# Kernel tuning notes

Measured on AMD Instinct MI355X. Metric: run time of the kernel, lower is better.

Reference implementation:

```python
import jax, jax.numpy as jnp
import numpy as np

N, E, DN, DE, H, L = 2048, 32768, 512, 512, 8, 2
BN_EPS = 1e-5  # torch BatchNorm1d eps; eval mode with running_mean=0, running_var=1


def setup_inputs():
    key = jax.random.key(0)
    ks = jax.random.split(key, 12)
    rng = np.random.default_rng(0)
    # unique directed edges: 3E/4 upper-triangular pairs + reverses of the first E/4
    iu, ju = np.triu_indices(N, k=1)
    sel = rng.choice(iu.size, size=3 * E // 4, replace=False)
    s, d = iu[sel], ju[sel]
    src = np.concatenate([s, d[: E // 4]])
    dst = np.concatenate([d, s[: E // 4]])
    edge_index = jnp.asarray(np.stack([src, dst]).astype(np.int32))

    def p(k, shape, fan_in):
        return jax.random.normal(k, shape, jnp.float32) / np.sqrt(fan_in).astype(np.float32)

    return dict(
        x=jax.random.normal(ks[0], (N, DN), jnp.float32),
        edge_feature=jax.random.normal(ks[1], (E, DE), jnp.float32),
        node_pos=jax.random.uniform(ks[2], (N, 3), jnp.float32) * 10.0,
        inw=p(ks[3], (L, 3 * DN, DN), DN),          # MHA in_proj_weight per layer
        inb=jnp.zeros((L, 3 * DN), jnp.float32),
        ow=p(ks[4], (L, DN, DN), DN),               # MHA out_proj
        ob=jnp.zeros((L, DN), jnp.float32),
        etw=p(ks[5], (L, DE, DE), DE),              # edge_transform Linear
        etb=jnp.zeros((L, DE), jnp.float32),
        etg=jnp.ones((L, DE), jnp.float32),         # edge_transform BN gamma
        etbb=jnp.zeros((L, DE), jnp.float32),       # edge_transform BN beta
        unw=p(ks[6], (L, DN, DN + DE), DN + DE),    # update_node Linear
        unb=jnp.zeros((L, DN), jnp.float32),
        uew=p(ks[7], (L, DE, 2 * DN + 2 * DE), 2 * DN + 2 * DE),  # update_edge Linear
        ueb=jnp.zeros((L, DE), jnp.float32),
        edge_index=edge_index,
    )


def _forward(x, edge_feature, node_pos, inw, inb, ow, ob, etw, etb, etg, etbb, unw, unb, uew, ueb, edge_index):
    src, dst = edge_index[0], edge_index[1]
    n, e = x.shape[0], src.shape[0]
    hd = DN // H
    # vectorized reverse-edge lookup (mirrors the torch edge_dict)
    keys = src * n + dst
    rkeys = dst * n + src
    order = jnp.argsort(keys)
    sk = keys[order]
    pos = jnp.clip(jnp.searchsorted(sk, rkeys), 0, e - 1)
    found = sk[pos] == rkeys
    rev_idx = order[pos]
    # distance-based attention mask: -inf everywhere, 1/(dist+eps) on (symmetric) edges, 1.0 on diagonal
    diff = node_pos[src] - node_pos[dst]
    w = 1.0 / (jnp.sqrt(jnp.sum(diff * diff, axis=-1)) + 1e-6)
    mask = jnp.full((n, n), -jnp.inf, x.dtype)
    mask = mask.at[src, dst].set(w).at[dst, src].set(w)
    diag = jnp.arange(n)
    mask = mask.at[diag, diag].set(1.0)
    bn_scale = np.float32(1.0 / np.sqrt(1.0 + BN_EPS))
    nf, ef = x, edge_feature
    for l in range(L):
        rev = jnp.where(found[:, None], ef[rev_idx], 0.0)
        # MHSA over all nodes as one sequence (batch=1), eval mode (dropout off)
        qkv = nf @ inw[l].T + inb[l]
        q, k, v = [t.reshape(n, H, hd) for t in jnp.split(qkv, 3, axis=-1)]
        scores = jnp.einsum('nhd,mhd->hnm', q * np.float32(1.0 / np.sqrt(hd)), k) + mask
        attn = jax.nn.softmax(scores, axis=-1)
        ctx = jnp.einsum('hnm,mhd->nhd', attn, v).reshape(n, DN)
        x_upd = ctx @ ow[l].T + ob[l]
        # message: update_edge on [x_i, e, e_rev, x_j] (flow=target_to_source -> x_i = x[src])
        upd_edge = jnp.concatenate([nf[src], ef, rev, nf[dst]], axis=1) @ uew[l].T + ueb[l]
        # edge_transform = Linear + BN(eval) + ReLU
        te = jax.nn.relu((ef @ etw[l].T + etb[l]) * bn_scale * etg[l] + etbb[l])
        # scatter-max to subject/object nodes (empty segments -> 0, torch_scatter convention)
        subj = jax.ops.segment_max(te, src, num_segments=n)
        obj = jax.ops.segment_max(te, dst, num_segments=n)
        subj = jnp.where(jnp.isneginf(subj), 0.0, subj)
        obj = jnp.where(jnp.isneginf(obj), 0.0, obj)
        nf = jnp.concatenate([x_upd, subj + obj], axis=1) @ unw[l].T + unb[l]
        ef = upd_edge
        if l < L - 1 or L == 1:
            nf = jax.nn.relu(nf)
            ef = jax.nn.relu(ef)
    return nf, ef


def reference(x, edge_feature, node_pos, inw, inb, ow, ob, etw, etb, etg, etbb, unw, unb, uew, ueb, edge_index):
    return _forward(x, edge_feature, node_pos, inw, inb, ow, ob, etw, etb, etg, etbb, unw, unb, uew, ueb, edge_index)
```

## Files before the change

kernel.cpp:

```cpp
#include <hip/hip_runtime.h>
#include <hip/hip_bf16.h>

#define NN 2048
#define EE 32768
#define DND 512
#define NH 8
#define HD 64
#define MAXD 128
#define NEGF (-1e30f)
#define BN_SCALE 0.9999950000374997f

typedef __attribute__((ext_vector_type(8))) short bf16x8;
typedef __attribute__((ext_vector_type(4))) float f32x4;
typedef unsigned short u16;
typedef unsigned int u32;

static __device__ __forceinline__ float4 ld4(const float* p) {
    return *reinterpret_cast<const float4*>(p);
}
static __device__ __forceinline__ u16 f2b(float f) {
    __hip_bfloat16 h = __float2bfloat16(f);
    return *reinterpret_cast<u16*>(&h);
}
static __device__ __forceinline__ float b2f(u32 bits) {
    return __uint_as_float(bits << 16);
}
static __device__ __forceinline__ void gl_lds(const u16* g, u16* l) {
    __builtin_amdgcn_global_load_lds((const __attribute__((address_space(1))) void*)g,
                                     (__attribute__((address_space(3))) void*)l, 16, 0, 0);
}


__global__ __launch_bounds__(256) void setup_init_k(int* __restrict__ t,
                                                    int* __restrict__ adj, float* __restrict__ wadj,
                                                    int* __restrict__ cnt,
                                                    int* __restrict__ ocnt, int* __restrict__ icnt,
                                                    u16* __restrict__ zero)
{
    int i = blockIdx.x * 256 + threadIdx.x;
    t[i] = -1;
    if (i < NN) {
        cnt[i] = 1; adj[i * MAXD] = i; wadj[i * MAXD] = 1.0f;
        ocnt[i] = 0; icnt[i] = 0;
    }
    if (i < 1024) zero[i] = 0;
}

__global__ __launch_bounds__(256) void fill_scatter_k(const int* __restrict__ ei, int* __restrict__ t,
                                                      int* __restrict__ oadj, int* __restrict__ ocnt,
                                                      int* __restrict__ iadj, int* __restrict__ icnt)
{
    int e = blockIdx.x * 256 + threadIdx.x;
    if (e >= EE) return;
    int s = ei[e], d = ei[EE + e];
    t[(size_t)s * NN + d] = e;
    int slot = atomicAdd(&ocnt[s], 1);
    if (slot < MAXD) oadj[s * MAXD + slot] = e;
    slot = atomicAdd(&icnt[d], 1);
    if (slot < MAXD) iadj[d * MAXD + slot] = e;
}

__global__ __launch_bounds__(256) void rev_csr_k(const int* __restrict__ ei, const int* __restrict__ t,
                                                 const float* __restrict__ pos,
                                                 int* __restrict__ rev,
                                                 int* __restrict__ adj, float* __restrict__ wadj,
                                                 int* __restrict__ cnt)
{
    int e = blockIdx.x * 256 + threadIdx.x;
    if (e >= EE) return;
    int s = ei[e], d = ei[EE + e];
    int r = t[(size_t)d * NN + s];
    rev[e] = r;
    float dx = pos[s * 3 + 0] - pos[d * 3 + 0];
    float dy = pos[s * 3 + 1] - pos[d * 3 + 1];
    float dz = pos[s * 3 + 2] - pos[d * 3 + 2];
    float w = 1.0f / (sqrtf(dx * dx + dy * dy + dz * dz) + 1e-6f);
    int slot = atomicAdd(&cnt[s], 1);
    if (slot < MAXD) { adj[s * MAXD + slot] = d; wadj[s * MAXD + slot] = w; }
    if (r < 0) {
        slot = atomicAdd(&cnt[d], 1);
        if (slot < MAXD) { adj[d * MAXD + slot] = s; wadj[d * MAXD + slot] = w; }
    }
}

__global__ __launch_bounds__(256) void conv_all_k(
    const float* __restrict__ x, const float* __restrict__ inw, const float* __restrict__ ow,
    const float* __restrict__ etw, const float* __restrict__ unw, const float* __restrict__ uew,
    const float* __restrict__ efin, u16* __restrict__ dst)
{
    size_t i = ((size_t)blockIdx.x * 256 + threadIdx.x) * 8;
    const float* s;
    size_t off;
    if (i < 1048576)      { s = x;    off = i; }
    else if (i < 2621440) { s = inw;  off = i - 1048576; }
    else if (i < 3145728) { s = ow;   off = i - 2621440; }
    else if (i < 3670016) { s = etw;  off = i - 3145728; }
    else if (i < 4718592) { s = unw;  off = i - 3670016; }
    else if (i < 6815744) { s = uew;  off = i - 4718592; }
    else                  { s = efin; off = i - 6815744; }
    float4 a = ld4(s + off), b = ld4(s + off + 4);
    u16 o[8];
    o[0] = f2b(a.x); o[1] = f2b(a.y); o[2] = f2b(a.z); o[3] = f2b(a.w);
    o[4] = f2b(b.x); o[5] = f2b(b.y); o[6] = f2b(b.z); o[7] = f2b(b.w);
    *reinterpret_cast<int4*>(dst + i) = *reinterpret_cast<const int4*>(o);
}

__global__ __launch_bounds__(256) void gather_max_k(const u16* __restrict__ te,
                                                    const int* __restrict__ oadj, const int* __restrict__ ocnt,
                                                    const int* __restrict__ iadj, const int* __restrict__ icnt,
                                                    u16* __restrict__ sums)
{
    const int i = blockIdx.x;
    const int c2 = threadIdx.x;
    float ms0 = 0.f, ms1 = 0.f, mo0 = 0.f, mo1 = 0.f;
    int no = ocnt[i]; if (no > MAXD) no = MAXD;
    for (int s = 0; s < no; ++s) {
        const int e = oadj[i * MAXD + s];
        const u32 v = *reinterpret_cast<const u32*>(te + (size_t)e * DND + c2 * 2);
        ms0 = fmaxf(ms0, b2f(v & 0xffffu));
        ms1 = fmaxf(ms1, b2f(v >> 16));
    }
    int ni = icnt[i]; if (ni > MAXD) ni = MAXD;
    for (int s = 0; s < ni; ++s) {
        const int e = iadj[i * MAXD + s];
        const u32 v = *reinterpret_cast<const u32*>(te + (size_t)e * DND + c2 * 2);
        mo0 = fmaxf(mo0, b2f(v & 0xffffu));
        mo1 = fmaxf(mo1, b2f(v >> 16));
    }
    const u32 r = (u32)f2b(ms0 + mo0) | ((u32)f2b(ms1 + mo1) << 16);
    *reinterpret_cast<u32*>(sums + (size_t)i * DND + c2 * 2) = r;
}

template <int MODE, int EPI, int WF32, int WBF16, int GY>
__global__ __launch_bounds__(256) void mgemm_k(
    const u16* __restrict__ WS, u32 a_off, u32 b_off, const float* __restrict__ bias,
    float* __restrict__ Cf, u16* __restrict__ Cb, int M, int Nc, int K,
    u32 g0_off, u32 g1_off, u32 gz_off,
    const int* __restrict__ srcv, const int* __restrict__ dstv, const int* __restrict__ revv,
    const float* __restrict__ eg, const float* __restrict__ eb)
{
    __shared__ u16 As2[2][8192];
    __shared__ u16 Bs2[2][8192];
    const int tid = threadIdx.x, lane = tid & 63, w = tid >> 6;
    const int wr = w >> 1, wc = w & 1;
    const int b = blockIdx.x;
    const int xcd = b & 7, kb = b >> 3;
    const int bm = ((kb / GY) * 8 + xcd) * 128;
    const int bn = (kb % GY) * 128;

    const int rl = lane >> 3;
    const u32 lx = (u32)(((lane & 7) ^ rl) * 8);

    u32 offA0[4], offA1[4], offB[4];
#pragma unroll
    for (int q = 0; q < 4; ++q) {
        const int ra = bm + w * 32 + q * 8 + rl;
        if (MODE == 0) {
            offA0[q] = a_off + (u32)ra * (u32)K + lx;
        } else {
            offA0[q] = g0_off + (u32)ra * 512u + lx;
            offA1[q] = g1_off + (u32)ra * 512u + lx;
        }
        offB[q] = b_off + (u32)(bn + w * 32 + q * 8 + rl) * (u32)K + lx;
    }

    const int nks = K >> 6;
    const int kq = lane >> 4, li = lane & 15;

    auto stage = [&](int t, int buf) {
        const u32 k0 = (u32)t * 64u;
        const int seg = (MODE == 0) ? 0 : (int)(k0 >> 9);
#pragma unroll
        for (int q = 0; q < 4; ++q) {
            u32 oa = (MODE == 0) ? offA0[q] : (seg == 0 ? offA0[q] : offA1[q]);
            const u32 koff = (MODE == 0) ? k0 : (k0 & 511u);
            gl_lds(WS + oa + koff, &As2[buf][(w * 32 + q * 8) * 64]);
        }
#pragma unroll
        for (int q = 0; q < 4; ++q)
            gl_lds(WS + offB[q] + k0, &Bs2[buf][(w * 32 + q * 8) * 64]);
    };

    f32x4 acc[4][4] = {};
    const int baseA = (wr * 64 + li) * 64 + ((kq ^ (li & 7)) * 8);
    const int baseB = (wc * 64 + li) * 64 + ((kq ^ (li & 7)) * 8);

    stage(0, 0);
    for (int t = 0; t < nks; ++t) {
        const int cur = t & 1;
        if (t + 1 < nks) stage(t + 1, cur ^ 1);
        if (t + 1 < nks) asm volatile("s_waitcnt vmcnt(8)" ::: "memory");
        else             asm volatile("s_waitcnt vmcnt(0)" ::: "memory");
        __builtin_amdgcn_s_barrier();
        __builtin_amdgcn_sched_barrier(0);
#pragma unroll
        for (int sub = 0; sub < 2; ++sub) {
            const int sx = sub << 5;
            bf16x8 af[4], bf[4];
#pragma unroll
            for (int m = 0; m < 4; ++m)
                af[m] = *reinterpret_cast<const bf16x8*>(&As2[cur][(baseA + m * 1024) ^ sx]);
#pragma unroll
            for (int n = 0; n < 4; ++n)
                bf[n] = *reinterpret_cast<const bf16x8*>(&Bs2[cur][(baseB + n * 1024) ^ sx]);
#pragma unroll
            for (int m = 0; m < 4; ++m)
#pragma unroll
                for (int n = 0; n < 4; ++n)
                    acc[m][n] = __builtin_amdgcn_mfma_f32_16x16x32_bf16(af[m], bf[n], acc[m][n], 0, 0, 0);
        }
        __builtin_amdgcn_s_barrier();
        __builtin_amdgcn_sched_barrier(0);
    }

    float bsv[4], scv[4], shv[4];
#pragma unroll
    for (int n = 0; n < 4; ++n) {
        const int col = bn + wc * 64 + n * 16 + li;
        bsv[n] = bias[col];
        if (EPI == 2) { scv[n] = BN_SCALE * eg[col]; shv[n] = eb[col]; }
    }
#pragma unroll
    for (int m = 0; m < 4; ++m) {
#pragma unroll
        for (int n = 0; n < 4; ++n) {
            const int col = bn + wc * 64 + n * 16 + li;
#pragma unroll
            for (int i = 0; i < 4; ++i) {
                float v = acc[m][n][i] + bsv[n];
                if (EPI == 2) v = fmaxf(fmaf(v, scv[n], shv[n]), 0.f);
                else if (EPI == 1) v = fmaxf(v, 0.f);
                const int r = bm + wr * 64 + m * 16 + (lane >> 4) * 4 + i;
                if (WF32) Cf[(size_t)r * Nc + col] = v;
                if (WBF16) Cb[(size_t)r * Nc + col] = f2b(v);
            }
        }
    }
}

template <int MODE, int EPI, int WF32, int WBF16>
__global__ __launch_bounds__(512, 2) void mgemm256_k(
    const u16* __restrict__ WS, u32 a_off, u32 b_off, const float* __restrict__ bias,
    float* __restrict__ Cf, u16* __restrict__ Cb, int M, int Nc, int K,
    u32 g0_off, u32 g1_off, u32 gz_off,
    const int* __restrict__ srcv, const int* __restrict__ dstv, const int* __restrict__ revv,
    const float* __restrict__ eg, const float* __restrict__ eb)
{
    __shared__ u16 SB[65536];
    const int tid = threadIdx.x, lane = tid & 63, w = tid >> 6;
    const int wr = w >> 2, wc = w & 3;
    const int b = blockIdx.x;
    const int bm = ((b & 7) + 8 * (b >> 4)) * 256;
    const int bn = ((b >> 3) & 1) * 256;

    const int rl = lane >> 3;
    const u32 lx = (u32)(((lane & 7) ^ rl) * 8);

    u32 offA0[4], offA1[4], offA2[4], offA3[4], offB[4];
#pragma unroll
    for (int q = 0; q < 4; ++q) {
        const int ra = bm + w * 32 + q * 8 + rl;
        if (MODE == 0) {
            offA0[q] = a_off + (u32)ra * (u32)K + lx;
        } else {
            offA0[q] = g0_off + (u32)srcv[ra] * 512u + lx;
            offA1[q] = g1_off + (u32)ra * 512u + lx;
            const int rv = revv[ra];
            offA2[q] = (rv >= 0 ? g1_off + (u32)rv * 512u : gz_off) + lx;
            offA3[q] = g0_off + (u32)dstv[ra] * 512u + lx;
        }
        offB[q] = b_off + (u32)(bn + w * 32 + q * 8 + rl) * (u32)K + lx;
    }

    const int nks = K >> 6;
    const int kq = lane >> 4, li = lane & 15;

    auto stageA2 = [&](int t, int buf, int q0) {
        const u32 k0 = (u32)t * 64u;
        const int seg = (MODE == 0) ? 0 : (int)(k0 >> 9);
        const u32 koff = (MODE == 0) ? k0 : (k0 & 511u);
#pragma unroll
        for (int q = q0; q < q0 + 2; ++q) {
            u32 oa;
            if (MODE == 0) oa = offA0[q];
            else           oa = (seg == 0 ? offA0[q] : seg == 1 ? offA1[q] : seg == 2 ? offA2[q] : offA3[q]);
            gl_lds(WS + oa + koff, &SB[buf * 16384 + (w * 32 + q * 8) * 64]);
        }
    };
    auto stageB2 = [&](int t, int buf, int q0) {
        const u32 k0 = (u32)t * 64u;
#pragma unroll
        for (int q = q0; q < q0 + 2; ++q)
            gl_lds(WS + offB[q] + k0, &SB[32768 + buf * 16384 + (w * 32 + q * 8) * 64]);
    };

    f32x4 acc[8][4] = {};
    const int baseA = (wr * 128 + li) * 64 + ((kq ^ (li & 7)) * 8);
    const int baseB = (wc * 64 + li) * 64 + ((kq ^ (li & 7)) * 8);

    stageA2(0, 0, 0); stageA2(0, 0, 2); stageB2(0, 0, 0); stageB2(0, 0, 2);
    for (int t = 0; t < nks; ++t) {
        const int cur = t & 1;
        const bool pf = (t + 1 < nks);
        if (pf) {
            stageA2(t + 1, cur ^ 1, 0);
            asm volatile("s_waitcnt vmcnt(2)" ::: "memory");
        } else {
            asm volatile("s_waitcnt vmcnt(0)" ::: "memory");
        }
        __builtin_amdgcn_s_barrier();
        __builtin_amdgcn_sched_barrier(0);
#pragma unroll
        for (int sub = 0; sub < 2; ++sub) {
            const int sx = sub << 5;
            bf16x8 bf[4];
#pragma unroll
            for (int n = 0; n < 4; ++n)
                bf[n] = *reinterpret_cast<const bf16x8*>(&SB[(32768 + cur * 16384 + baseB + n * 1024) ^ sx]);
#pragma unroll
            for (int mh = 0; mh < 2; ++mh) {
                if (pf) {
                    if (sub == 0 && mh == 0)      stageA2(t + 1, cur ^ 1, 2);
                    else if (sub == 0 && mh == 1) stageB2(t + 1, cur ^ 1, 0);
                    else if (sub == 1 && mh == 0) stageB2(t + 1, cur ^ 1, 2);
                }
                bf16x8 af[4];
#pragma unroll
                for (int m = 0; m < 4; ++m)
                    af[m] = *reinterpret_cast<const bf16x8*>(&SB[(cur * 16384 + baseA + (mh * 4 + m) * 1024) ^ sx]);
                __builtin_amdgcn_sched_barrier(0);
                __builtin_amdgcn_s_setprio(1);
#pragma unroll
                for (int m = 0; m < 4; ++m)
#pragma unroll
                    for (int n = 0; n < 4; ++n)
                        acc[mh * 4 + m][n] =
                            __builtin_amdgcn_mfma_f32_16x16x32_bf16(af[m], bf[n], acc[mh * 4 + m][n], 0, 0, 0);
                __builtin_amdgcn_s_setprio(0);
                __builtin_amdgcn_sched_barrier(0);
            }
        }
        __builtin_amdgcn_s_barrier();
        __builtin_amdgcn_sched_barrier(0);
    }

    float bsv[4], scv[4], shv[4];
#pragma unroll
    for (int n = 0; n < 4; ++n) {
        const int col = bn + wc * 64 + n * 16 + li;
        bsv[n] = bias[col];
        if (EPI == 2) { scv[n] = BN_SCALE * eg[col]; shv[n] = eb[col]; }
    }
#pragma unroll
    for (int m = 0; m < 8; ++m) {
#pragma unroll
        for (int n = 0; n < 4; ++n) {
            const int col = bn + wc * 64 + n * 16 + li;
#pragma unroll
            for (int i = 0; i < 4; ++i) {
                float v = acc[m][n][i] + bsv[n];
                if (EPI == 2) v = fmaxf(fmaf(v, scv[n], shv[n]), 0.f);
                else if (EPI == 1) v = fmaxf(v, 0.f);
                const int r = bm + wr * 128 + m * 16 + (lane >> 4) * 4 + i;
                if (WF32) Cf[(size_t)r * Nc + col] = v;
                if (WBF16) Cb[(size_t)r * Nc + col] = f2b(v);
            }
        }
    }
}

__global__ __launch_bounds__(256) void attn_sp_k(const u16* __restrict__ qkvb,
                                                 const int* __restrict__ adj,
                                                 const float* __restrict__ wadj,
                                                 const int* __restrict__ cnt,
                                                 u16* __restrict__ ctxb)
{
    const int i = blockIdx.x;
    const int wv = threadIdx.x >> 6, lane = threadIdx.x & 63;
    const int h = blockIdx.y * 4 + wv;
    __shared__ float qs[4][64];
    qs[wv][lane] = b2f((u32)qkvb[(size_t)i * 1536 + h * HD + lane]) * 0.125f;
    __syncthreads();
    int deg = cnt[i];
    if (deg > MAXD) deg = MAXD;
    float m = -3.0e38f, lsum = 0.f, c = 0.f;
    for (int base = 0; base < deg; base += 64) {
        int nn_ = deg - base; if (nn_ > 64) nn_ = 64;
        int j = 0;
        float s = NEGF;
        if (lane < nn_) {
            j = adj[i * MAXD + base + lane];
            const float wgt = wadj[i * MAXD + base + lane];
            const u16* kr = qkvb + (size_t)j * 1536 + DND + h * HD;
            float accd = 0.f;
#pragma unroll
            for (int cq = 0; cq < 4; ++cq) {
                uint4 kv = *reinterpret_cast<const uint4*>(kr + cq * 16);
                const float* qp = &qs[wv][cq * 16];
                accd = fmaf(qp[0],  b2f(kv.x & 0xffffu), accd);
                accd = fmaf(qp[1],  b2f(kv.x >> 16), accd);
                accd = fmaf(qp[2],  b2f(kv.y & 0xffffu), accd);
                accd = fmaf(qp[3],  b2f(kv.y >> 16), accd);
                accd = fmaf(qp[4],  b2f(kv.z & 0xffffu), accd);
                accd = fmaf(qp[5],  b2f(kv.z >> 16), accd);
                accd = fmaf(qp[6],  b2f(kv.w & 0xffffu), accd);
                accd = fmaf(qp[7],  b2f(kv.w >> 16), accd);
                uint4 kv2 = *reinterpret_cast<const uint4*>(kr + cq * 16 + 8);
                accd = fmaf(qp[8],  b2f(kv2.x & 0xffffu), accd);
                accd = fmaf(qp[9],  b2f(kv2.x >> 16), accd);
                accd = fmaf(qp[10], b2f(kv2.y & 0xffffu), accd);
                accd = fmaf(qp[11], b2f(kv2.y >> 16), accd);
                accd = fmaf(qp[12], b2f(kv2.z & 0xffffu), accd);
                accd = fmaf(qp[13], b2f(kv2.z >> 16), accd);
                accd = fmaf(qp[14], b2f(kv2.w & 0xffffu), accd);
                accd = fmaf(qp[15], b2f(kv2.w >> 16), accd);
            }
            s = accd + wgt;
        }
        float mloc = s;
#pragma unroll
        for (int o = 1; o < 64; o <<= 1) mloc = fmaxf(mloc, __shfl_xor(mloc, o, 64));
        const float mnew = fmaxf(m, mloc);
        const float alpha = __expf(m - mnew);
        const float p = (lane < nn_) ? __expf(s - mnew) : 0.f;
        float ps = p;
#pragma unroll
        for (int o = 1; o < 64; o <<= 1) ps += __shfl_xor(ps, o, 64);
        lsum = lsum * alpha + ps;
        c *= alpha;
        for (int l = 0; l < nn_; ++l) {
            const float pj = __shfl(p, l, 64);
            const int jj = __shfl(j, l, 64);
            c = fmaf(pj, b2f((u32)qkvb[(size_t)jj * 1536 + 2 * DND + h * HD + lane]), c);
        }
        m = mnew;
    }
    ctxb[(size_t)i * DND + h * HD + lane] = f2b(c / lsum);
}

extern "C" void kernel_launch(void* const* d_in, const int* in_sizes, int n_in,
                              void* d_out, int out_size, void* d_ws, size_t ws_size,
                              hipStream_t stream)
{
    const float* x    = (const float*)d_in[0];
    const float* efin = (const float*)d_in[1];
    const float* pos  = (const float*)d_in[2];
    const float* inw  = (const float*)d_in[3];
    const float* inb  = (const float*)d_in[4];
    const float* ow   = (const float*)d_in[5];
    const float* ob   = (const float*)d_in[6];
    const float* etw  = (const float*)d_in[7];
    const float* etb  = (const float*)d_in[8];
    const float* etg  = (const float*)d_in[9];
    const float* etbb = (const float*)d_in[10];
    const float* unw  = (const float*)d_in[11];
    const float* unb  = (const float*)d_in[12];
    const float* uew  = (const float*)d_in[13];
    const float* ueb  = (const float*)d_in[14];
    const int*   ei   = (const int*)d_in[15];

    float* W = (float*)d_ws;
    u16*   qkvb  = (u16*)W;
    u16*   te    = (u16*)W;
    int*   rev   = (int*)(W + 8388608);
    u16*   zero  = (u16*)(W + 8421376);
    int*   adj   = (int*)(W + 8421888);
    float* wadj  = W + 8684032;
    int*   cnt   = (int*)(W + 8946176);
    int*   oadj  = (int*)(W + 8948224);
    int*   ocnt  = (int*)(W + 9210368);
    int*   iadj  = (int*)(W + 9212416);
    int*   icnt  = (int*)(W + 9474560);
    u16*   ctxb  = (u16*)(W + 9476608);
    u16*   xupdb = (u16*)(W + 10000896);
    u16*   sums  = (u16*)(W + 10525184);
    u16*   nfb   = (u16*)(W + 11049472);
    u16*   wbf   = (u16*)(W + 11573760);
    u16*   efbA  = (u16*)(W + 14457344);
    u16*   efbB  = (u16*)(W + 22845952);
    int*   table = (int*)efbA;

    u16* inwb = wbf;
    u16* owb  = wbf + 1572864;
    u16* etwb = wbf + 2097152;
    u16* unwb = wbf + 2621440;
    u16* uewb = wbf + 3670016;

    float* out_nf = (float*)d_out;
    float* out_ef = out_nf + (size_t)NN * DND;

    const int* srcv = ei;
    const int* dstv = ei + EE;

    const u16* WSu = (const u16*)d_ws;
    auto uoff = [&](const void* p) { return (u32)((const u16*)p - WSu); };

    setup_init_k<<<NN * NN / 256, 256, 0, stream>>>(table, adj, wadj, cnt, ocnt, icnt, zero);
    fill_scatter_k<<<EE / 256, 256, 0, stream>>>(ei, table, oadj, ocnt, iadj, icnt);
    rev_csr_k<<<EE / 256, 256, 0, stream>>>(ei, table, pos, rev, adj, wadj, cnt);
    conv_all_k<<<11520, 256, 0, stream>>>(x, inw, ow, etw, unw, uew, efin, nfb);

    for (int l = 0; l < 2; ++l) {
        const u16* efb_cur = l ? efbB : efbA;
        const u16* inwb_l = inwb + (size_t)l * 786432;
        const u16* owb_l  = owb  + (size_t)l * 262144;
        const u16* etwb_l = etwb + (size_t)l * 262144;
        const u16* unwb_l = unwb + (size_t)l * 524288;
        const u16* uewb_l = uewb + (size_t)l * 1048576;
        const float* inb_l  = inb  + (size_t)l * 1536;
        const float* ob_l   = ob   + (size_t)l * 512;
        const float* etb_l  = etb  + (size_t)l * 512;
        const float* etg_l  = etg  + (size_t)l * 512;
        const float* etbb_l = etbb + (size_t)l * 512;
        const float* unb_l  = unb  + (size_t)l * 512;
        const float* ueb_l  = ueb  + (size_t)l * 512;

        mgemm_k<0, 0, 0, 1, 12><<<192, 256, 0, stream>>>(
            WSu, uoff(nfb), uoff(inwb_l), inb_l, nullptr, qkvb, NN, 1536, DND,
            0, 0, 0, nullptr, nullptr, nullptr, nullptr, nullptr);

        attn_sp_k<<<dim3(NN, 2), 256, 0, stream>>>(qkvb, adj, wadj, cnt, ctxb);

        mgemm_k<0, 0, 0, 1, 4><<<64, 256, 0, stream>>>(
            WSu, uoff(ctxb), uoff(owb_l), ob_l, nullptr, xupdb, NN, DND, DND,
            0, 0, 0, nullptr, nullptr, nullptr, nullptr, nullptr);

        mgemm256_k<0, 2, 0, 1><<<256, 512, 0, stream>>>(
            WSu, uoff(efb_cur), uoff(etwb_l), etb_l, nullptr, te, EE, DND, DND,
            0, 0, 0, nullptr, nullptr, nullptr, etg_l, etbb_l);

        gather_max_k<<<NN, 256, 0, stream>>>(te, oadj, ocnt, iadj, icnt, sums);

        if (l == 0)
            mgemm256_k<1, 1, 0, 1><<<256, 512, 0, stream>>>(
                WSu, 0, uoff(uewb_l), ueb_l, nullptr, efbB, EE, DND, 2048,
                uoff(nfb), uoff(efb_cur), uoff(zero), srcv, dstv, rev, nullptr, nullptr);
        else
            mgemm256_k<1, 0, 1, 0><<<256, 512, 0, stream>>>(
                WSu, 0, uoff(uewb_l), ueb_l, out_ef, nullptr, EE, DND, 2048,
                uoff(nfb), uoff(efb_cur), uoff(zero), srcv, dstv, rev, nullptr, nullptr);

        if (l == 0)
            mgemm_k<2, 1, 0, 1, 4><<<64, 256, 0, stream>>>(
                WSu, 0, uoff(unwb_l), unb_l, nullptr, nfb, NN, DND, 1024,
                uoff(xupdb), uoff(sums), 0, nullptr, nullptr, nullptr, nullptr, nullptr);
        else
            mgemm_k<2, 0, 1, 0, 4><<<64, 256, 0, stream>>>(
                WSu, 0, uoff(unwb_l), unb_l, out_nf, nullptr, NN, DND, 1024,
                uoff(xupdb), uoff(sums), 0, nullptr, nullptr, nullptr, nullptr, nullptr);
    }
}
```

Measured before the change: 431.2 us.

## Fold attention out-projection into update_node weights and shrink edge lookup table

Multiplies the x-part of each layer's update_node weight by the out_proj weight once per call, and folds the out_proj bias into a combined bias. The node update GEMM can then read the attention context directly, which removes the separate out_proj GEMM and its intermediate buffer in both layers. The dense reverse-edge lookup table now stores 16-bit edge ids, halving the N×N initialisation and scatter traffic. In exchange there are new small setup kernels (a weight transpose, a fused weight GEMM, a bias dot-product and a copy), and the fused weight is rounded to bf16 after the product, which changes numerics slightly.

Measured after the change: 462.5 us. +7.3%, slower.

```diff
diff --git a/kernel.cpp b/kernel.cpp
--- a/kernel.cpp
+++ b/kernel.cpp
@@ -31,14 +31,14 @@
 }
 
 
-__global__ __launch_bounds__(256) void setup_init_k(int* __restrict__ t,
+__global__ __launch_bounds__(256) void setup_init_k(u32* __restrict__ t2,
                                                     int* __restrict__ adj, float* __restrict__ wadj,
                                                     int* __restrict__ cnt,
                                                     int* __restrict__ ocnt, int* __restrict__ icnt,
                                                     u16* __restrict__ zero)
 {
     int i = blockIdx.x * 256 + threadIdx.x;
-    t[i] = -1;
+    t2[i] = 0xFFFFFFFFu;
     if (i < NN) {
         cnt[i] = 1; adj[i * MAXD] = i; wadj[i * MAXD] = 1.0f;
         ocnt[i] = 0; icnt[i] = 0;
@@ -46,21 +46,21 @@
     if (i < 1024) zero[i] = 0;
 }
 
-__global__ __launch_bounds__(256) void fill_scatter_k(const int* __restrict__ ei, int* __restrict__ t,
+__global__ __launch_bounds__(256) void fill_scatter_k(const int* __restrict__ ei, u16* __restrict__ t,
                                                       int* __restrict__ oadj, int* __restrict__ ocnt,
                                                       int* __restrict__ iadj, int* __restrict__ icnt)
 {
     int e = blockIdx.x * 256 + threadIdx.x;
     if (e >= EE) return;
     int s = ei[e], d = ei[EE + e];
-    t[(size_t)s * NN + d] = e;
+    t[(size_t)s * NN + d] = (u16)e;
     int slot = atomicAdd(&ocnt[s], 1);
     if (slot < MAXD) oadj[s * MAXD + slot] = e;
     slot = atomicAdd(&icnt[d], 1);
     if (slot < MAXD) iadj[d * MAXD + slot] = e;
 }
 
-__global__ __launch_bounds__(256) void rev_csr_k(const int* __restrict__ ei, const int* __restrict__ t,
+__global__ __launch_bounds__(256) void rev_csr_k(const int* __restrict__ ei, const u16* __restrict__ t,
                                                  const float* __restrict__ pos,
                                                  int* __restrict__ rev,
                                                  int* __restrict__ adj, float* __restrict__ wadj,
@@ -69,7 +69,8 @@
     int e = blockIdx.x * 256 + threadIdx.x;
     if (e >= EE) return;
     int s = ei[e], d = ei[EE + e];
-    int r = t[(size_t)d * NN + s];
+    u16 r16 = t[(size_t)d * NN + s];
+    int r = (r16 == 0xFFFFu) ? -1 : (int)r16;
     rev[e] = r;
     float dx = pos[s * 3 + 0] - pos[d * 3 + 0];
     float dy = pos[s * 3 + 1] - pos[d * 3 + 1];
@@ -84,25 +85,49 @@
 }
 
 __global__ __launch_bounds__(256) void conv_all_k(
-    const float* __restrict__ x, const float* __restrict__ inw, const float* __restrict__ ow,
+    const float* __restrict__ x, const float* __restrict__ inw,
     const float* __restrict__ etw, const float* __restrict__ unw, const float* __restrict__ uew,
     const float* __restrict__ efin, u16* __restrict__ dst)
 {
     size_t i = ((size_t)blockIdx.x * 256 + threadIdx.x) * 8;
     const float* s;
-    size_t off;
+    size_t off, dsto = i;
     if (i < 1048576)      { s = x;    off = i; }
     else if (i < 2621440) { s = inw;  off = i - 1048576; }
-    else if (i < 3145728) { s = ow;   off = i - 2621440; }
-    else if (i < 3670016) { s = etw;  off = i - 3145728; }
-    else if (i < 4718592) { s = unw;  off = i - 3670016; }
-    else if (i < 6815744) { s = uew;  off = i - 4718592; }
-    else                  { s = efin; off = i - 6815744; }
+    else if (i < 3145728) { s = etw;  off = i - 2621440; }
+    else if (i < 4194304) { s = unw;  off = i - 3145728; }
+    else if (i < 6291456) { s = uew;  off = i - 4194304; }
+    else                  { s = efin; off = i - 6291456; dsto = i + 524288; }
     float4 a = ld4(s + off), b = ld4(s + off + 4);
     u16 o[8];
     o[0] = f2b(a.x); o[1] = f2b(a.y); o[2] = f2b(a.z); o[3] = f2b(a.w);
     o[4] = f2b(b.x); o[5] = f2b(b.y); o[6] = f2b(b.z); o[7] = f2b(b.w);
-    *reinterpret_cast<int4*>(dst + i) = *reinterpret_cast<const int4*>(o);
+    *reinterpret_cast<int4*>(dst + dsto) = *reinterpret_cast<const int4*>(o);
+}
+
+__global__ __launch_bounds__(256) void owT_k(const float* __restrict__ ow, u16* __restrict__ owTb) {
+    int i8 = (blockIdx.x * 256 + threadIdx.x) * 8;
+    int l = i8 >> 18, rem = i8 & 262143;
+    int k = rem >> 9, j0 = rem & 511;
+    const float* src = ow + (size_t)l * 262144;
+    u16 o[8];
+#pragma unroll
+    for (int tjj = 0; tjj < 8; ++tjj) o[tjj] = f2b(src[(size_t)(j0 + tjj) * 512 + k]);
+    *reinterpret_cast<int4*>(owTb + i8) = *reinterpret_cast<const int4*>(o);
+}
+
+__global__ __launch_bounds__(256) void biasp_k(const float* __restrict__ unw, const float* __restrict__ ob,
+                                               const float* __restrict__ unb, float* __restrict__ biasp) {
+    int idx = blockIdx.x * 256 + threadIdx.x;
+    int l = idx >> 9, c = idx & 511;
+    const float* row = unw + (size_t)l * 524288 + (size_t)c * 1024;
+    const float* obl = ob + l * 512;
+    float s = unb[idx];
+    for (int j = 0; j < 512; j += 4) {
+        float4 a = ld4(row + j), b = ld4(obl + j);
+        s += a.x * b.x + a.y * b.y + a.z * b.z + a.w * b.w;
+    }
+    biasp[idx] = s;
 }
 
 __global__ __launch_bounds__(256) void gather_max_k(const u16* __restrict__ te,
@@ -131,12 +156,11 @@
     *reinterpret_cast<u32*>(sums + (size_t)i * DND + c2 * 2) = r;
 }
 
-template <int MODE, int EPI, int WF32, int WBF16, int GY>
+template <int MODE, int EPI, int WF32, int WBF16, int GY, int SWZ>
 __global__ __launch_bounds__(256) void mgemm_k(
-    const u16* __restrict__ WS, u32 a_off, u32 b_off, const float* __restrict__ bias,
+    const u16* __restrict__ WS, u32 a_off, u32 a_stride, u32 b_off, const float* __restrict__ bias,
     float* __restrict__ Cf, u16* __restrict__ Cb, int M, int Nc, int K,
-    u32 g0_off, u32 g1_off, u32 gz_off,
-    const int* __restrict__ srcv, const int* __restrict__ dstv, const int* __restrict__ revv,
+    u32 g0_off, u32 g1_off,
     const float* __restrict__ eg, const float* __restrict__ eb)
 {
     __shared__ u16 As2[2][8192];
@@ -144,9 +168,15 @@
     const int tid = threadIdx.x, lane = tid & 63, w = tid >> 6;
     const int wr = w >> 1, wc = w & 1;
     const int b = blockIdx.x;
-    const int xcd = b & 7, kb = b >> 3;
-    const int bm = ((kb / GY) * 8 + xcd) * 128;
-    const int bn = (kb % GY) * 128;
+    int bm, bn;
+    if (SWZ) {
+        const int xcd = b & 7, kb = b >> 3;
+        bm = ((kb / GY) * 8 + xcd) * 128;
+        bn = (kb % GY) * 128;
+    } else {
+        bm = (b / GY) * 128;
+        bn = (b % GY) * 128;
+    }
 
     const int rl = lane >> 3;
     const u32 lx = (u32)(((lane & 7) ^ rl) * 8);
@@ -156,7 +186,7 @@
     for (int q = 0; q < 4; ++q) {
         const int ra = bm + w * 32 + q * 8 + rl;
         if (MODE == 0) {
-            offA0[q] = a_off + (u32)ra * (u32)K + lx;
+            offA0[q] = a_off + (u32)ra * a_stride + lx;
         } else {
             offA0[q] = g0_off + (u32)ra * 512u + lx;
             offA1[q] = g1_off + (u32)ra * 512u + lx;
@@ -472,19 +502,20 @@
     int*   iadj  = (int*)(W + 9212416);
     int*   icnt  = (int*)(W + 9474560);
     u16*   ctxb  = (u16*)(W + 9476608);
-    u16*   xupdb = (u16*)(W + 10000896);
+    u16*   newWb = (u16*)(W + 10000896);
     u16*   sums  = (u16*)(W + 10525184);
     u16*   nfb   = (u16*)(W + 11049472);
     u16*   wbf   = (u16*)(W + 11573760);
     u16*   efbA  = (u16*)(W + 14457344);
     u16*   efbB  = (u16*)(W + 22845952);
-    int*   table = (int*)efbA;
+    float* biasp = W + 31234560;
+    u16*   table = (u16*)efbA;
 
     u16* inwb = wbf;
-    u16* owb  = wbf + 1572864;
-    u16* etwb = wbf + 2097152;
-    u16* unwb = wbf + 2621440;
-    u16* uewb = wbf + 3670016;
+    u16* etwb = wbf + 1572864;
+    u16* unwb = wbf + 2097152;
+    u16* uewb = wbf + 3145728;
+    u16* owTb = wbf + 5242880;
 
     float* out_nf = (float*)d_out;
     float* out_ef = out_nf + (size_t)NN * DND;
@@ -495,35 +526,41 @@
     const u16* WSu = (const u16*)d_ws;
     auto uoff = [&](const void* p) { return (u32)((const u16*)p - WSu); };
 
-    setup_init_k<<<NN * NN / 256, 256, 0, stream>>>(table, adj, wadj, cnt, ocnt, icnt, zero);
+    setup_init_k<<<NN * NN / 512, 256, 0, stream>>>((u32*)table, adj, wadj, cnt, ocnt, icnt, zero);
     fill_scatter_k<<<EE / 256, 256, 0, stream>>>(ei, table, oadj, ocnt, iadj, icnt);
     rev_csr_k<<<EE / 256, 256, 0, stream>>>(ei, table, pos, rev, adj, wadj, cnt);
-    conv_all_k<<<11520, 256, 0, stream>>>(x, inw, ow, etw, unw, uew, efin, nfb);
+    conv_all_k<<<11264, 256, 0, stream>>>(x, inw, etw, unw, uew, efin, nfb);
+    owT_k<<<256, 256, 0, stream>>>(ow, owTb);
+    for (int l = 0; l < 2; ++l)
+        mgemm_k<0, 0, 0, 1, 4, 0><<<16, 256, 0, stream>>>(
+            WSu, uoff(unwb) + (u32)l * 524288u, 1024u, uoff(owTb) + (u32)l * 262144u, (const float*)zero,
+            nullptr, newWb + (size_t)l * 524288, 512, 1024, 512, 0, 0, nullptr, nullptr);
+    biasp_k<<<4, 256, 0, stream>>>(unw, ob, unb, biasp);
+    {
+        struct {} _;
+    }
+
+    extern void __global__ cp_unw1_k(const u16*, u16*);
+    cp_unw1_k<<<512, 256, 0, stream>>>(unwb, newWb);
 
     for (int l = 0; l < 2; ++l) {
         const u16* efb_cur = l ? efbB : efbA;
         const u16* inwb_l = inwb + (size_t)l * 786432;
-        const u16* owb_l  = owb  + (size_t)l * 262144;
         const u16* etwb_l = etwb + (size_t)l * 262144;
-        const u16* unwb_l = unwb + (size_t)l * 524288;
         const u16* uewb_l = uewb + (size_t)l * 1048576;
+        const u16* newWb_l = newWb + (size_t)l * 524288;
         const float* inb_l  = inb  + (size_t)l * 1536;
-        const float* ob_l   = ob   + (size_t)l * 512;
         const float* etb_l  = etb  + (size_t)l * 512;
         const float* etg_l  = etg  + (size_t)l * 512;
         const float* etbb_l = etbb + (size_t)l * 512;
-        const float* unb_l  = unb  + (size_t)l * 512;
+        const float* biasp_l = biasp + (size_t)l * 512;
         const float* ueb_l  = ueb  + (size_t)l * 512;
 
-        mgemm_k<0, 0, 0, 1, 12><<<192, 256, 0, stream>>>(
-            WSu, uoff(nfb), uoff(inwb_l), inb_l, nullptr, qkvb, NN, 1536, DND,
-            0, 0, 0, nullptr, nullptr, nullptr, nullptr, nullptr);
+        mgemm_k<0, 0, 0, 1, 12, 1><<<192, 256, 0, stream>>>(
+            WSu, uoff(nfb), 512u, uoff(inwb_l), inb_l, nullptr, qkvb, NN, 1536, DND,
+            0, 0, nullptr, nullptr);
 
         attn_sp_k<<<dim3(NN, 2), 256, 0, stream>>>(qkvb, adj, wadj, cnt, ctxb);
-
-        mgemm_k<0, 0, 0, 1, 4><<<64, 256, 0, stream>>>(
-            WSu, uoff(ctxb), uoff(owb_l), ob_l, nullptr, xupdb, NN, DND, DND,
-            0, 0, 0, nullptr, nullptr, nullptr, nullptr, nullptr);
 
         mgemm256_k<0, 2, 0, 1><<<256, 512, 0, stream>>>(
             WSu, uoff(efb_cur), uoff(etwb_l), etb_l, nullptr, te, EE, DND, DND,
@@ -541,12 +578,20 @@
                 uoff(nfb), uoff(efb_cur), uoff(zero), srcv, dstv, rev, nullptr, nullptr);
 
         if (l == 0)
-            mgemm_k<2, 1, 0, 1, 4><<<64, 256, 0, stream>>>(
-                WSu, 0, uoff(unwb_l), unb_l, nullptr, nfb, NN, DND, 1024,
-                uoff(xupdb), uoff(sums), 0, nullptr, nullptr, nullptr, nullptr, nullptr);
+            mgemm_k<2, 1, 0, 1, 4, 1><<<64, 256, 0, stream>>>(
+                WSu, 0, 0u, uoff(newWb_l), biasp_l, nullptr, nfb, NN, DND, 1024,
+                uoff(ctxb), uoff(sums), nullptr, nullptr);
         else
-            mgemm_k<2, 0, 1, 0, 4><<<64, 256, 0, stream>>>(
-                WSu, 0, uoff(unwb_l), unb_l, out_nf, nullptr, NN, DND, 1024,
-                uoff(xupdb), uoff(sums), 0, nullptr, nullptr, nullptr, nullptr, nullptr);
-    }
-}
+            mgemm_k<2, 0, 1, 0, 4, 1><<<64, 256, 0, stream>>>(
+                WSu, 0, 0u, uoff(newWb_l), biasp_l, out_nf, nullptr, NN, DND, 1024,
+                uoff(ctxb), uoff(sums), nullptr, nullptr);
+    }
+}
+
+__global__ __launch_bounds__(256) void cp_unw1_k(const u16* __restrict__ unwb, u16* __restrict__ newWb) {
+    int i8 = (blockIdx.x * 256 + threadIdx.x) * 8;
+    int l = i8 >> 18, rem = i8 & 262143;
+    int r = rem >> 9, k = rem & 511;
+    size_t off = (size_t)l * 524288 + (size_t)r * 1024 + 512 + k;
+    *reinterpret_cast<int4*>(newWb + off) = *reinterpret_cast<const int4*>(unwb + off);
+}
```
